# Optimization experiments

Measured on AMD Instinct MI355X. Metric: run time of the kernel, lower is better.

Reference implementation:

```python
import jax, jax.numpy as jnp
import numpy as np

B, N, G, E = 4, 8192, 512, 512
D = 3 * E  # fused channel dim = 1536
BN_EPS = 1e-5


def setup_inputs() -> dict:
    key = jax.random.key(0)
    ks = jax.random.split(key, 8)
    f32 = jnp.float32
    return {
        "xyz": jax.random.normal(ks[0], (B, N, 3), f32),
        "centers": jax.random.normal(ks[1], (B, G, 3), f32),
        "H4": jax.random.normal(ks[2], (B, G, E), f32),
        "H8": jax.random.normal(ks[3], (B, G, E), f32),
        "H12": jax.random.normal(ks[4], (B, G, E), f32),
        "w1": jax.random.normal(ks[5], (512, D), f32) * 0.02,
        "b1": jnp.zeros((512,), f32),
        "g1": jnp.ones((512,), f32),
        "be1": jnp.zeros((512,), f32),
        "m1": jnp.zeros((512,), f32),
        "v1": jnp.ones((512,), f32),
        "w2": jax.random.normal(ks[6], (512, 512), f32) * 0.02,
        "b2": jnp.zeros((512,), f32),
        "g2": jnp.ones((512,), f32),
        "be2": jnp.zeros((512,), f32),
        "m2": jnp.zeros((512,), f32),
        "v2": jnp.ones((512,), f32),
    }


def _bn(x, gamma, beta, mean, var):
    # BatchNorm1d, eval mode with running stats (per-channel, last axis)
    return (x - mean) * jax.lax.rsqrt(var + BN_EPS) * gamma + beta


def reference(xyz, centers, H4, H8, H12,
              w1, b1, g1, be1, m1, v1,
              w2, b2, g2, be2, m2, v2):
    fused = jnp.concatenate([H4, H8, H12], axis=-1)  # [B,G,D]
    # squared pairwise distances [B,N,G]
    d = (jnp.sum(xyz * xyz, axis=-1, keepdims=True)
         + jnp.sum(centers * centers, axis=-1)[:, None, :]
         - 2.0 * jnp.einsum('bnc,bgc->bng', xyz, centers))
    neg_d3, idx = jax.lax.top_k(-d, 3)  # 3 smallest distances, ascending
    d3 = -neg_d3  # [B,N,3]
    recip = 1.0 / (d3 + 1e-8)
    w = recip / jnp.sum(recip, axis=-1, keepdims=True)  # [B,N,3]
    # gather neighbor features: [B,N,3,D]
    gathered = jax.vmap(lambda f, i: f[i])(fused, idx)
    interp = jnp.einsum('bnk,bnkd->bnd', w, gathered)  # [B,N,D]
    # 1x1 conv == per-point linear; conv -> BN(eval) -> ReLU, twice
    h = jax.nn.relu(_bn(interp @ w1.T + b1, g1, be1, m1, v1))
    h = jax.nn.relu(_bn(h @ w2.T + b2, g2, be2, m2, v2))
    return h  # [B,N,512]
```

## Files before the change

kernel.cpp:

```cpp
#include <hip/hip_runtime.h>
#include <hip/hip_cooperative_groups.h>
#include <stdint.h>

#define NP 8192
#define NG 512
#define DF 1536

namespace cg = cooperative_groups;

using f32x4    = __attribute__((ext_vector_type(4))) float;
using bf16x8   = __attribute__((ext_vector_type(8))) __bf16;
using ushort8v = __attribute__((ext_vector_type(8))) unsigned short;


__device__ __forceinline__ unsigned short f32_to_bf16(float f) {
  unsigned int u = __float_as_uint(f);
  u += 0x7fffu + ((u >> 16) & 1u);
  return (unsigned short)(u >> 16);
}
__device__ __forceinline__ float bf2f(unsigned short u) {
  return __uint_as_float(((unsigned)u) << 16);
}

struct FusedArgs {
  const float *xyz, *centers, *H4, *H8, *H12, *w1, *w2;
  const float *g1, *be1, *m1, *v1, *g2, *be2, *m2, *v2, *b1, *b2;
  unsigned short *fswz, *w1s, *w2s, *Amatb;
  int *nidx; float *nw, *s1, *t1, *s2, *t2;
  float *outp;
};

__device__ void phase_setup(const FusedArgs& a, char* smem, int w) {
  const int tid = threadIdx.x;
  if (w < 512) {
    float4* cs = (float4*)smem;
    const int b = w >> 7;
    for (int i = tid; i < NG; i += 256) {
      float c0 = a.centers[((size_t)b * NG + i) * 3 + 0];
      float c1 = a.centers[((size_t)b * NG + i) * 3 + 1];
      float c2 = a.centers[((size_t)b * NG + i) * 3 + 2];
      float4 v; v.x = c0; v.y = c1; v.z = c2; v.w = c0 * c0 + c1 * c1 + c2 * c2;
      cs[(i >> 7) * 129 + (i & 127)] = v;
    }
    __syncthreads();
    const int t = (w & 127) * 256 + tid;
    const int p = t >> 2, q = t & 3;
    const size_t pi = (size_t)b * NP + p;
    const float x0 = a.xyz[pi * 3 + 0], x1 = a.xyz[pi * 3 + 1], x2 = a.xyz[pi * 3 + 2];
    const float xx = x0 * x0 + x1 * x1 + x2 * x2;
    float d0 = 3.4e38f, d1 = 3.4e38f, d2 = 3.4e38f;
    int i0 = 0, i1 = 0, i2 = 0;
    const int gbase = q * 128;
    const float4* csq = cs + q * 129;
#pragma unroll 4
    for (int j = 0; j < 128; ++j) {
      float4 c = csq[j];
      float d = xx + c.w - 2.0f * (x0 * c.x + x1 * c.y + x2 * c.z);
      int g = gbase + j;
      bool c0 = d < d0, c1 = d < d1, c2 = d < d2;
      float nd2 = c1 ? d1 : (c2 ? d : d2); int ni2 = c1 ? i1 : (c2 ? g : i2);
      float nd1 = c0 ? d0 : (c1 ? d : d1); int ni1 = c0 ? i0 : (c1 ? g : i1);
      d0 = c0 ? d : d0;                    i0 = c0 ? g : i0;
      d1 = nd1; i1 = ni1; d2 = nd2; i2 = ni2;
    }
#pragma unroll
    for (int off = 1; off <= 2; off <<= 1) {
      float e0 = __shfl_xor(d0, off), e1 = __shfl_xor(d1, off), e2 = __shfl_xor(d2, off);
      int j0 = __shfl_xor(i0, off), j1 = __shfl_xor(i1, off), j2 = __shfl_xor(i2, off);
#pragma unroll
      for (int s = 0; s < 3; ++s) {
        float e = (s == 0) ? e0 : (s == 1 ? e1 : e2);
        int   j = (s == 0) ? j0 : (s == 1 ? j1 : j2);
        bool c0 = (e < d0) || (e == d0 && j < i0);
        bool c1 = (e < d1) || (e == d1 && j < i1);
        bool c2 = (e < d2) || (e == d2 && j < i2);
        float nd2 = c1 ? d1 : (c2 ? e : d2); int ni2 = c1 ? i1 : (c2 ? j : i2);
        float nd1 = c0 ? d0 : (c1 ? e : d1); int ni1 = c0 ? i0 : (c1 ? j : i1);
        d0 = c0 ? e : d0;                    i0 = c0 ? j : i0;
        d1 = nd1; i1 = ni1; d2 = nd2; i2 = ni2;
      }
    }
    if (q == 0) {
      float r0 = 1.0f / (d0 + 1e-8f), r1 = 1.0f / (d1 + 1e-8f), r2 = 1.0f / (d2 + 1e-8f);
      float inv = 1.0f / (r0 + r1 + r2);
      a.nw[pi * 3 + 0] = r0 * inv; a.nw[pi * 3 + 1] = r1 * inv; a.nw[pi * 3 + 2] = r2 * inv;
      a.nidx[pi * 3 + 0] = i0; a.nidx[pi * 3 + 1] = i1; a.nidx[pi * 3 + 2] = i2;
    }
    __syncthreads();
  } else if (w < 2048) {
    const int qd = (w - 512) * 256 + tid;
    const int L = qd & 63, t2 = qd >> 6;
    const int kc = t2 % 48, mg = t2 / 48;
    const int m = mg * 16 + (L & 15);
    const int k = kc * 32 + (L >> 4) * 8;
    const float* src = (k < 512) ? a.H4 : (k < 1024 ? a.H8 : a.H12);
    const float* sp = &src[(size_t)m * 512 + (k & 511)];
    float4 va = *(const float4*)sp, vb = *(const float4*)(sp + 4);
    ushort8v o;
    o[0] = f32_to_bf16(va.x); o[1] = f32_to_bf16(va.y);
    o[2] = f32_to_bf16(va.z); o[3] = f32_to_bf16(va.w);
    o[4] = f32_to_bf16(vb.x); o[5] = f32_to_bf16(vb.y);
    o[6] = f32_to_bf16(vb.z); o[7] = f32_to_bf16(vb.w);
    *(ushort8v*)&a.fswz[((size_t)(mg * 48 + kc)) * 512 + L * 8] = o;
  } else if (w < 2432) {
    const int qd = (w - 2048) * 256 + tid;
    const int L = qd & 63, t2 = qd >> 6;
    const int kc = t2 % 48, ng = t2 / 48;
    const int n = ng * 16 + (L & 15);
    const int k = kc * 32 + (L >> 4) * 8;
    const float* sp = &a.w1[(size_t)n * 1536 + k];
    float4 va = *(const float4*)sp, vb = *(const float4*)(sp + 4);
    ushort8v o;
    o[0] = f32_to_bf16(va.x); o[1] = f32_to_bf16(va.y);
    o[2] = f32_to_bf16(va.z); o[3] = f32_to_bf16(va.w);
    o[4] = f32_to_bf16(vb.x); o[5] = f32_to_bf16(vb.y);
    o[6] = f32_to_bf16(vb.z); o[7] = f32_to_bf16(vb.w);
    *(ushort8v*)&a.w1s[((size_t)(ng * 48 + kc)) * 512 + L * 8] = o;
  } else if (w < 2560) {
    const int qd = (w - 2432) * 256 + tid;
    const int L = qd & 63, t2 = qd >> 6;
    const int kc = t2 & 15, ng = t2 >> 4;
    const int n = ng * 16 + (L & 15);
    const int k = kc * 32 + (L >> 4) * 8;
    const float* sp = &a.w2[(size_t)n * 512 + k];
    float4 va = *(const float4*)sp, vb = *(const float4*)(sp + 4);
    ushort8v o;
    o[0] = f32_to_bf16(va.x); o[1] = f32_to_bf16(va.y);
    o[2] = f32_to_bf16(va.z); o[3] = f32_to_bf16(va.w);
    o[4] = f32_to_bf16(vb.x); o[5] = f32_to_bf16(vb.y);
    o[6] = f32_to_bf16(vb.z); o[7] = f32_to_bf16(vb.w);
    *(ushort8v*)&a.w2s[((size_t)(ng * 16 + kc)) * 512 + L * 8] = o;
  } else {
    for (int i = tid; i < 512; i += 256) {
      float sa = a.g1[i] / sqrtf(a.v1[i] + 1e-5f);
      a.s1[i] = sa; a.t1[i] = a.be1[i] - a.m1[i] * sa;
      float sb = a.g2[i] / sqrtf(a.v2[i] + 1e-5f);
      a.s2[i] = sb; a.t2[i] = a.be2[i] - a.m2[i] * sb;
    }
  }
}

__device__ void phase_gemm1(const FusedArgs& a, char* smem) {
  float* red = (float*)smem;
  const int tid = threadIdx.x, lane = tid & 63, wv = tid >> 6;
  const int blk = blockIdx.x;
  const int m0 = (blk >> 3) * 32;
  const int n0 = (blk & 7) * 64;
  const unsigned short* Ap = a.fswz + ((size_t)(m0 >> 4) * 48 + wv * 12) * 512 + lane * 8;
  const unsigned short* Bp = a.w1s  + ((size_t)(n0 >> 4) * 48 + wv * 12) * 512 + lane * 8;

  f32x4 acc[2][4];
#pragma unroll
  for (int i = 0; i < 2; ++i)
#pragma unroll
    for (int j = 0; j < 4; ++j) acc[i][j] = (f32x4){0.f, 0.f, 0.f, 0.f};

  bf16x8 af[2], bfr[4], afn[2], bfn[4];
#pragma unroll
  for (int i = 0; i < 2; ++i)
    af[i]  = __builtin_bit_cast(bf16x8, *(const ushort8v*)(Ap + (size_t)i * 48 * 512));
#pragma unroll
  for (int i = 0; i < 4; ++i)
    bfr[i] = __builtin_bit_cast(bf16x8, *(const ushort8v*)(Bp + (size_t)i * 48 * 512));
#pragma unroll 1
  for (int kc = 0; kc < 12; ++kc) {
    if (kc < 11) {
#pragma unroll
      for (int i = 0; i < 2; ++i)
        afn[i] = __builtin_bit_cast(bf16x8, *(const ushort8v*)(Ap + (size_t)i * 48 * 512 + (kc + 1) * 512));
#pragma unroll
      for (int i = 0; i < 4; ++i)
        bfn[i] = __builtin_bit_cast(bf16x8, *(const ushort8v*)(Bp + (size_t)i * 48 * 512 + (kc + 1) * 512));
    }
#pragma unroll
    for (int mi = 0; mi < 2; ++mi)
#pragma unroll
      for (int ni = 0; ni < 4; ++ni)
        acc[mi][ni] = __builtin_amdgcn_mfma_f32_16x16x32_bf16(af[mi], bfr[ni], acc[mi][ni], 0, 0, 0);
#pragma unroll
    for (int i = 0; i < 2; ++i) af[i] = afn[i];
#pragma unroll
    for (int i = 0; i < 4; ++i) bfr[i] = bfn[i];
  }

  for (int w = 0; w < 4; ++w) {
    if (wv == w) {
#pragma unroll
      for (int mi = 0; mi < 2; ++mi)
#pragma unroll
        for (int ni = 0; ni < 4; ++ni) {
          int col = ni * 16 + (lane & 15);
#pragma unroll
          for (int r = 0; r < 4; ++r) {
            int row = mi * 16 + (lane >> 4) * 4 + r;
            if (w == 0) red[row * 65 + col] = acc[mi][ni][r];
            else        red[row * 65 + col] += acc[mi][ni][r];
          }
        }
    }
    __syncthreads();
  }
  const int row = tid >> 3;
  const int col = (tid & 7) * 8;
  ushort8v o;
#pragma unroll
  for (int j = 0; j < 8; ++j) {
    int n = n0 + col + j;
    float v = red[row * 65 + col + j];
    o[j] = f32_to_bf16(a.s1[n] * (v + a.b1[n]) + a.t1[n]);
  }
  *(ushort8v*)&a.Amatb[(size_t)(m0 + row) * 512 + n0 + col] = o;
  __syncthreads();
}

__device__ void phase_mega(const FusedArgs& a, char* smem) {
  unsigned short* hl = (unsigned short*)smem;
  const int tid = threadIdx.x, lane = tid & 63, wv = tid >> 6;
  const int xcd = blockIdx.x & 7, slot = blockIdx.x >> 3;
  const int m0 = (xcd * 64 + slot) * 64;

  {
    const int p = m0 + wv * 16 + (lane & 15);
    const int b = p >> 13;
    const int i0 = a.nidx[p * 3 + 0], i1 = a.nidx[p * 3 + 1], i2 = a.nidx[p * 3 + 2];
    const float w0 = a.nw[p * 3 + 0], w1v = a.nw[p * 3 + 1], w2v = a.nw[p * 3 + 2];
    const int co = (lane >> 4) * 8;
    const unsigned short* A0 = a.Amatb + ((size_t)(b * 512 + i0)) * 512 + co;
    const unsigned short* A1 = a.Amatb + ((size_t)(b * 512 + i1)) * 512 + co;
    const unsigned short* A2 = a.Amatb + ((size_t)(b * 512 + i2)) * 512 + co;
    unsigned short* wp = hl + (size_t)(wv * 16) * 512 + lane * 8;
#pragma unroll 4
    for (int kc = 0; kc < 16; ++kc) {
      ushort8v u0 = *(const ushort8v*)(A0 + kc * 32);
      ushort8v u1 = *(const ushort8v*)(A1 + kc * 32);
      ushort8v u2 = *(const ushort8v*)(A2 + kc * 32);
      ushort8v o;
#pragma unroll
      for (int j = 0; j < 8; ++j) {
        float v = w0 * bf2f(u0[j]) + w1v * bf2f(u1[j]) + w2v * bf2f(u2[j]);
        o[j] = f32_to_bf16(fmaxf(v, 0.f));
      }
      *(ushort8v*)(wp + (size_t)kc * 512) = o;
    }
  }
  __syncthreads();

  const int n0 = wv * 128;
  const unsigned short* Bbase = a.w2s + (size_t)(n0 >> 4) * 16 * 512 + lane * 8;

  f32x4 acc[4][8];
#pragma unroll
  for (int i = 0; i < 4; ++i)
#pragma unroll
    for (int j = 0; j < 8; ++j) acc[i][j] = (f32x4){0.f, 0.f, 0.f, 0.f};

#pragma unroll 1
  for (int kc = 0; kc < 16; ++kc) {
    bf16x8 af[4], bfr[8];
#pragma unroll
    for (int mi = 0; mi < 4; ++mi)
      af[mi] = __builtin_bit_cast(bf16x8,
          *(const ushort8v*)(hl + (size_t)(mi * 16 + kc) * 512 + lane * 8));
#pragma unroll
    for (int ni = 0; ni < 8; ++ni)
      bfr[ni] = __builtin_bit_cast(bf16x8,
          *(const ushort8v*)(Bbase + (size_t)(ni * 16 + kc) * 512));
#pragma unroll
    for (int mi = 0; mi < 4; ++mi)
#pragma unroll
      for (int ni = 0; ni < 8; ++ni)
        acc[mi][ni] = __builtin_amdgcn_mfma_f32_16x16x32_bf16(af[mi], bfr[ni], acc[mi][ni], 0, 0, 0);
  }

#pragma unroll
  for (int mi = 0; mi < 4; ++mi) {
    int mbase = m0 + mi * 16 + (lane >> 4) * 4;
#pragma unroll
    for (int ni = 0; ni < 8; ++ni) {
      int n = n0 + ni * 16 + (lane & 15);
      float s = a.s2[n], bb = a.b2[n], t = a.t2[n];
      f32x4 v = acc[mi][ni];
#pragma unroll
      for (int r = 0; r < 4; ++r)
        a.outp[(size_t)(mbase + r) * 512 + n] = fmaxf(s * (v[r] + bb) + t, 0.f);
    }
  }
}

__global__ __launch_bounds__(256, 2) void fused_kernel(FusedArgs a) {
  __shared__ __align__(16) char smem[65536];
  cg::grid_group grid = cg::this_grid();
  const int blk = blockIdx.x;
  for (int u = blk; u <= 2560; u += 512) phase_setup(a, smem, u);
  grid.sync();
  phase_gemm1(a, smem);
  grid.sync();
  phase_mega(a, smem);
}

__global__ __launch_bounds__(256) void k_setup(FusedArgs a) {
  __shared__ __align__(16) char smem[8448];
  for (int u = blockIdx.x; u <= 2560; u += 512) phase_setup(a, smem, u);
}
__global__ __launch_bounds__(256) void k_gemm1(FusedArgs a) {
  __shared__ __align__(16) char smem[8448];
  phase_gemm1(a, smem);
}
__global__ __launch_bounds__(256, 2) void k_mega(FusedArgs a) {
  __shared__ __align__(16) char smem[65536];
  phase_mega(a, smem);
}

extern "C" void kernel_launch(void* const* d_in, const int* in_sizes, int n_in,
                              void* d_out, int out_size, void* d_ws, size_t ws_size,
                              hipStream_t stream) {
  char* ws = (char*)d_ws;
  FusedArgs a;
  a.xyz     = (const float*)d_in[0];
  a.centers = (const float*)d_in[1];
  a.H4      = (const float*)d_in[2];
  a.H8      = (const float*)d_in[3];
  a.H12     = (const float*)d_in[4];
  a.w1      = (const float*)d_in[5];
  a.b1      = (const float*)d_in[6];
  a.g1      = (const float*)d_in[7];
  a.be1     = (const float*)d_in[8];
  a.m1      = (const float*)d_in[9];
  a.v1      = (const float*)d_in[10];
  a.w2      = (const float*)d_in[11];
  a.b2      = (const float*)d_in[12];
  a.g2      = (const float*)d_in[13];
  a.be2     = (const float*)d_in[14];
  a.m2      = (const float*)d_in[15];
  a.v2      = (const float*)d_in[16];
  a.fswz  = (unsigned short*)(ws);
  a.w1s   = (unsigned short*)(ws + 6291456);
  a.w2s   = (unsigned short*)(ws + 7864320);
  a.Amatb = (unsigned short*)(ws + 8388608);
  a.nidx  = (int*)           (ws + 10485760);
  a.nw    = (float*)         (ws + 10878976);
  a.s1    = (float*)         (ws + 11272192);
  a.t1 = a.s1 + 512; a.s2 = a.t1 + 512; a.t2 = a.s2 + 512;
  a.outp  = (float*)d_out;

  int nb = 0;
  hipError_t qerr = hipOccupancyMaxActiveBlocksPerMultiprocessor(
      &nb, reinterpret_cast<const void*>(fused_kernel), 256, 0);
  bool coop_ok = (qerr == hipSuccess) && (nb >= 2);
  if (coop_ok) {
    void* kp[] = { (void*)&a };
    hipError_t lerr = hipLaunchCooperativeKernel(
        (const void*)fused_kernel, dim3(512), dim3(256), kp, 0, stream);
    coop_ok = (lerr == hipSuccess);
  }
  if (!coop_ok) {
    k_setup <<<512, 256, 0, stream>>>(a);
    k_gemm1 <<<512, 256, 0, stream>>>(a);
    k_mega  <<<512, 256, 0, stream>>>(a);
  }
}
```

Before: 167.5 us.

## Overlap kNN with GEMM1 and double grid to 1024 blocks with smaller mega tiles

Moves the kNN search out of the setup phase so it runs alongside the first GEMM in a second phase, with each half of a 1024-block cooperative grid taking one of the two. The mega phase now handles 32 rows per block instead of 64, which halves its shared memory and accumulator footprint so launch bounds can ask for 4 blocks per CU. The cast work is spread over more blocks. The aim is to cut phase imbalance and raise occupancy. The cost is that each block reloads the W2 tiles for fewer rows, and 4 blocks per CU may push register pressure or fail the cooperative occupancy check, which would fall back to three separate launches.

```diff
diff --git a/kernel.cpp b/kernel.cpp
--- a/kernel.cpp
+++ b/kernel.cpp
@@ -11,6 +11,7 @@
 using f32x4    = __attribute__((ext_vector_type(4))) float;
 using bf16x8   = __attribute__((ext_vector_type(8))) __bf16;
 using ushort8v = __attribute__((ext_vector_type(8))) unsigned short;
+using ushort4v = __attribute__((ext_vector_type(4))) unsigned short;
 
 
 __device__ __forceinline__ unsigned short f32_to_bf16(float f) {
@@ -30,65 +31,68 @@
   float *outp;
 };
 
-__device__ void phase_setup(const FusedArgs& a, char* smem, int w) {
+__device__ void phase_knn(const FusedArgs& a, char* smem, int w) {
   const int tid = threadIdx.x;
-  if (w < 512) {
-    float4* cs = (float4*)smem;
-    const int b = w >> 7;
-    for (int i = tid; i < NG; i += 256) {
-      float c0 = a.centers[((size_t)b * NG + i) * 3 + 0];
-      float c1 = a.centers[((size_t)b * NG + i) * 3 + 1];
-      float c2 = a.centers[((size_t)b * NG + i) * 3 + 2];
-      float4 v; v.x = c0; v.y = c1; v.z = c2; v.w = c0 * c0 + c1 * c1 + c2 * c2;
-      cs[(i >> 7) * 129 + (i & 127)] = v;
-    }
-    __syncthreads();
-    const int t = (w & 127) * 256 + tid;
-    const int p = t >> 2, q = t & 3;
-    const size_t pi = (size_t)b * NP + p;
-    const float x0 = a.xyz[pi * 3 + 0], x1 = a.xyz[pi * 3 + 1], x2 = a.xyz[pi * 3 + 2];
-    const float xx = x0 * x0 + x1 * x1 + x2 * x2;
-    float d0 = 3.4e38f, d1 = 3.4e38f, d2 = 3.4e38f;
-    int i0 = 0, i1 = 0, i2 = 0;
-    const int gbase = q * 128;
-    const float4* csq = cs + q * 129;
+  float4* cs = (float4*)smem;
+  const int b = w >> 7;
+  for (int i = tid; i < NG; i += 256) {
+    float c0 = a.centers[((size_t)b * NG + i) * 3 + 0];
+    float c1 = a.centers[((size_t)b * NG + i) * 3 + 1];
+    float c2 = a.centers[((size_t)b * NG + i) * 3 + 2];
+    float4 v; v.x = c0; v.y = c1; v.z = c2; v.w = c0 * c0 + c1 * c1 + c2 * c2;
+    cs[(i >> 7) * 129 + (i & 127)] = v;
+  }
+  __syncthreads();
+  const int t = (w & 127) * 256 + tid;
+  const int p = t >> 2, q = t & 3;
+  const size_t pi = (size_t)b * NP + p;
+  const float x0 = a.xyz[pi * 3 + 0], x1 = a.xyz[pi * 3 + 1], x2 = a.xyz[pi * 3 + 2];
+  const float xx = x0 * x0 + x1 * x1 + x2 * x2;
+  float d0 = 3.4e38f, d1 = 3.4e38f, d2 = 3.4e38f;
+  int i0 = 0, i1 = 0, i2 = 0;
+  const int gbase = q * 128;
+  const float4* csq = cs + q * 129;
 #pragma unroll 4
-    for (int j = 0; j < 128; ++j) {
-      float4 c = csq[j];
-      float d = xx + c.w - 2.0f * (x0 * c.x + x1 * c.y + x2 * c.z);
-      int g = gbase + j;
-      bool c0 = d < d0, c1 = d < d1, c2 = d < d2;
-      float nd2 = c1 ? d1 : (c2 ? d : d2); int ni2 = c1 ? i1 : (c2 ? g : i2);
-      float nd1 = c0 ? d0 : (c1 ? d : d1); int ni1 = c0 ? i0 : (c1 ? g : i1);
-      d0 = c0 ? d : d0;                    i0 = c0 ? g : i0;
+  for (int j = 0; j < 128; ++j) {
+    float4 c = csq[j];
+    float d = xx + c.w - 2.0f * (x0 * c.x + x1 * c.y + x2 * c.z);
+    int g = gbase + j;
+    bool c0 = d < d0, c1 = d < d1, c2 = d < d2;
+    float nd2 = c1 ? d1 : (c2 ? d : d2); int ni2 = c1 ? i1 : (c2 ? g : i2);
+    float nd1 = c0 ? d0 : (c1 ? d : d1); int ni1 = c0 ? i0 : (c1 ? g : i1);
+    d0 = c0 ? d : d0;                    i0 = c0 ? g : i0;
+    d1 = nd1; i1 = ni1; d2 = nd2; i2 = ni2;
+  }
+#pragma unroll
+  for (int off = 1; off <= 2; off <<= 1) {
+    float e0 = __shfl_xor(d0, off), e1 = __shfl_xor(d1, off), e2 = __shfl_xor(d2, off);
+    int j0 = __shfl_xor(i0, off), j1 = __shfl_xor(i1, off), j2 = __shfl_xor(i2, off);
+#pragma unroll
+    for (int s = 0; s < 3; ++s) {
+      float e = (s == 0) ? e0 : (s == 1 ? e1 : e2);
+      int   j = (s == 0) ? j0 : (s == 1 ? j1 : j2);
+      bool c0 = (e < d0) || (e == d0 && j < i0);
+      bool c1 = (e < d1) || (e == d1 && j < i1);
+      bool c2 = (e < d2) || (e == d2 && j < i2);
+      float nd2 = c1 ? d1 : (c2 ? e : d2); int ni2 = c1 ? i1 : (c2 ? j : i2);
+      float nd1 = c0 ? d0 : (c1 ? e : d1); int ni1 = c0 ? i0 : (c1 ? j : i1);
+      d0 = c0 ? e : d0;                    i0 = c0 ? j : i0;
       d1 = nd1; i1 = ni1; d2 = nd2; i2 = ni2;
     }
-#pragma unroll
-    for (int off = 1; off <= 2; off <<= 1) {
-      float e0 = __shfl_xor(d0, off), e1 = __shfl_xor(d1, off), e2 = __shfl_xor(d2, off);
-      int j0 = __shfl_xor(i0, off), j1 = __shfl_xor(i1, off), j2 = __shfl_xor(i2, off);
-#pragma unroll
-      for (int s = 0; s < 3; ++s) {
-        float e = (s == 0) ? e0 : (s == 1 ? e1 : e2);
-        int   j = (s == 0) ? j0 : (s == 1 ? j1 : j2);
-        bool c0 = (e < d0) || (e == d0 && j < i0);
-        bool c1 = (e < d1) || (e == d1 && j < i1);
-        bool c2 = (e < d2) || (e == d2 && j < i2);
-        float nd2 = c1 ? d1 : (c2 ? e : d2); int ni2 = c1 ? i1 : (c2 ? j : i2);
-        float nd1 = c0 ? d0 : (c1 ? e : d1); int ni1 = c0 ? i0 : (c1 ? j : i1);
-        d0 = c0 ? e : d0;                    i0 = c0 ? j : i0;
-        d1 = nd1; i1 = ni1; d2 = nd2; i2 = ni2;
-      }
-    }
-    if (q == 0) {
-      float r0 = 1.0f / (d0 + 1e-8f), r1 = 1.0f / (d1 + 1e-8f), r2 = 1.0f / (d2 + 1e-8f);
-      float inv = 1.0f / (r0 + r1 + r2);
-      a.nw[pi * 3 + 0] = r0 * inv; a.nw[pi * 3 + 1] = r1 * inv; a.nw[pi * 3 + 2] = r2 * inv;
-      a.nidx[pi * 3 + 0] = i0; a.nidx[pi * 3 + 1] = i1; a.nidx[pi * 3 + 2] = i2;
-    }
-    __syncthreads();
-  } else if (w < 2048) {
-    const int qd = (w - 512) * 256 + tid;
+  }
+  if (q == 0) {
+    float r0 = 1.0f / (d0 + 1e-8f), r1 = 1.0f / (d1 + 1e-8f), r2 = 1.0f / (d2 + 1e-8f);
+    float inv = 1.0f / (r0 + r1 + r2);
+    a.nw[pi * 3 + 0] = r0 * inv; a.nw[pi * 3 + 1] = r1 * inv; a.nw[pi * 3 + 2] = r2 * inv;
+    a.nidx[pi * 3 + 0] = i0; a.nidx[pi * 3 + 1] = i1; a.nidx[pi * 3 + 2] = i2;
+  }
+  __syncthreads();
+}
+
+__device__ void phase_casts(const FusedArgs& a, int u) {
+  const int tid = threadIdx.x;
+  if (u < 2048) {
+    const int qd = (u - 512) * 256 + tid;
     const int L = qd & 63, t2 = qd >> 6;
     const int kc = t2 % 48, mg = t2 / 48;
     const int m = mg * 16 + (L & 15);
@@ -102,8 +106,8 @@
     o[4] = f32_to_bf16(vb.x); o[5] = f32_to_bf16(vb.y);
     o[6] = f32_to_bf16(vb.z); o[7] = f32_to_bf16(vb.w);
     *(ushort8v*)&a.fswz[((size_t)(mg * 48 + kc)) * 512 + L * 8] = o;
-  } else if (w < 2432) {
-    const int qd = (w - 2048) * 256 + tid;
+  } else if (u < 2432) {
+    const int qd = (u - 2048) * 256 + tid;
     const int L = qd & 63, t2 = qd >> 6;
     const int kc = t2 % 48, ng = t2 / 48;
     const int n = ng * 16 + (L & 15);
@@ -116,8 +120,8 @@
     o[4] = f32_to_bf16(vb.x); o[5] = f32_to_bf16(vb.y);
     o[6] = f32_to_bf16(vb.z); o[7] = f32_to_bf16(vb.w);
     *(ushort8v*)&a.w1s[((size_t)(ng * 48 + kc)) * 512 + L * 8] = o;
-  } else if (w < 2560) {
-    const int qd = (w - 2432) * 256 + tid;
+  } else if (u < 2560) {
+    const int qd = (u - 2432) * 256 + tid;
     const int L = qd & 63, t2 = qd >> 6;
     const int kc = t2 & 15, ng = t2 >> 4;
     const int n = ng * 16 + (L & 15);
@@ -140,10 +144,9 @@
   }
 }
 
-__device__ void phase_gemm1(const FusedArgs& a, char* smem) {
+__device__ void phase_gemm1(const FusedArgs& a, char* smem, int blk) {
   float* red = (float*)smem;
   const int tid = threadIdx.x, lane = tid & 63, wv = tid >> 6;
-  const int blk = blockIdx.x;
   const int m0 = (blk >> 3) * 32;
   const int n0 = (blk & 7) * 64;
   const unsigned short* Ap = a.fswz + ((size_t)(m0 >> 4) * 48 + wv * 12) * 512 + lane * 8;
@@ -217,30 +220,31 @@
   unsigned short* hl = (unsigned short*)smem;
   const int tid = threadIdx.x, lane = tid & 63, wv = tid >> 6;
   const int xcd = blockIdx.x & 7, slot = blockIdx.x >> 3;
-  const int m0 = (xcd * 64 + slot) * 64;
+  const int m0 = (xcd * 128 + slot) * 32;
 
   {
-    const int p = m0 + wv * 16 + (lane & 15);
+    const int rg = wv >> 1, kc0 = (wv & 1) * 8;
+    const int p = m0 + rg * 16 + (lane & 15);
     const int b = p >> 13;
     const int i0 = a.nidx[p * 3 + 0], i1 = a.nidx[p * 3 + 1], i2 = a.nidx[p * 3 + 2];
     const float w0 = a.nw[p * 3 + 0], w1v = a.nw[p * 3 + 1], w2v = a.nw[p * 3 + 2];
-    const int co = (lane >> 4) * 8;
+    const int co = kc0 * 32 + (lane >> 4) * 8;
     const unsigned short* A0 = a.Amatb + ((size_t)(b * 512 + i0)) * 512 + co;
     const unsigned short* A1 = a.Amatb + ((size_t)(b * 512 + i1)) * 512 + co;
     const unsigned short* A2 = a.Amatb + ((size_t)(b * 512 + i2)) * 512 + co;
-    unsigned short* wp = hl + (size_t)(wv * 16) * 512 + lane * 8;
+    unsigned short* wp = hl + (size_t)(rg * 16 + kc0) * 512 + lane * 8;
 #pragma unroll 4
-    for (int kc = 0; kc < 16; ++kc) {
-      ushort8v u0 = *(const ushort8v*)(A0 + kc * 32);
-      ushort8v u1 = *(const ushort8v*)(A1 + kc * 32);
-      ushort8v u2 = *(const ushort8v*)(A2 + kc * 32);
+    for (int j = 0; j < 8; ++j) {
+      ushort8v u0 = *(const ushort8v*)(A0 + j * 32);
+      ushort8v u1 = *(const ushort8v*)(A1 + j * 32);
+      ushort8v u2 = *(const ushort8v*)(A2 + j * 32);
       ushort8v o;
 #pragma unroll
-      for (int j = 0; j < 8; ++j) {
-        float v = w0 * bf2f(u0[j]) + w1v * bf2f(u1[j]) + w2v * bf2f(u2[j]);
-        o[j] = f32_to_bf16(fmaxf(v, 0.f));
+      for (int jj = 0; jj < 8; ++jj) {
+        float v = w0 * bf2f(u0[jj]) + w1v * bf2f(u1[jj]) + w2v * bf2f(u2[jj]);
+        o[jj] = f32_to_bf16(fmaxf(v, 0.f));
       }
-      *(ushort8v*)(wp + (size_t)kc * 512) = o;
+      *(ushort8v*)(wp + (size_t)j * 512) = o;
     }
   }
   __syncthreads();
@@ -248,32 +252,37 @@
   const int n0 = wv * 128;
   const unsigned short* Bbase = a.w2s + (size_t)(n0 >> 4) * 16 * 512 + lane * 8;
 
-  f32x4 acc[4][8];
-#pragma unroll
-  for (int i = 0; i < 4; ++i)
+  f32x4 acc[2][8];
+#pragma unroll
+  for (int i = 0; i < 2; ++i)
 #pragma unroll
     for (int j = 0; j < 8; ++j) acc[i][j] = (f32x4){0.f, 0.f, 0.f, 0.f};
 
 #pragma unroll 1
   for (int kc = 0; kc < 16; ++kc) {
-    bf16x8 af[4], bfr[8];
-#pragma unroll
-    for (int mi = 0; mi < 4; ++mi)
+    bf16x8 af[2];
+#pragma unroll
+    for (int mi = 0; mi < 2; ++mi)
       af[mi] = __builtin_bit_cast(bf16x8,
           *(const ushort8v*)(hl + (size_t)(mi * 16 + kc) * 512 + lane * 8));
 #pragma unroll
-    for (int ni = 0; ni < 8; ++ni)
-      bfr[ni] = __builtin_bit_cast(bf16x8,
-          *(const ushort8v*)(Bbase + (size_t)(ni * 16 + kc) * 512));
-#pragma unroll
-    for (int mi = 0; mi < 4; ++mi)
-#pragma unroll
-      for (int ni = 0; ni < 8; ++ni)
-        acc[mi][ni] = __builtin_amdgcn_mfma_f32_16x16x32_bf16(af[mi], bfr[ni], acc[mi][ni], 0, 0, 0);
-  }
-
-#pragma unroll
-  for (int mi = 0; mi < 4; ++mi) {
+    for (int h = 0; h < 2; ++h) {
+      bf16x8 bfr[4];
+#pragma unroll
+      for (int ni = 0; ni < 4; ++ni)
+        bfr[ni] = __builtin_bit_cast(bf16x8,
+            *(const ushort8v*)(Bbase + (size_t)((h * 4 + ni) * 16 + kc) * 512));
+#pragma unroll
+      for (int mi = 0; mi < 2; ++mi)
+#pragma unroll
+        for (int ni = 0; ni < 4; ++ni)
+          acc[mi][h * 4 + ni] = __builtin_amdgcn_mfma_f32_16x16x32_bf16(
+              af[mi], bfr[ni], acc[mi][h * 4 + ni], 0, 0, 0);
+    }
+  }
+
+#pragma unroll
+  for (int mi = 0; mi < 2; ++mi) {
     int mbase = m0 + mi * 16 + (lane >> 4) * 4;
 #pragma unroll
     for (int ni = 0; ni < 8; ++ni) {
@@ -287,27 +296,28 @@
   }
 }
 
-__global__ __launch_bounds__(256, 2) void fused_kernel(FusedArgs a) {
-  __shared__ __align__(16) char smem[65536];
+__global__ __launch_bounds__(256, 4) void fused_kernel(FusedArgs a) {
+  __shared__ __align__(16) char smem[32768];
   cg::grid_group grid = cg::this_grid();
   const int blk = blockIdx.x;
-  for (int u = blk; u <= 2560; u += 512) phase_setup(a, smem, u);
+  for (int u = 512 + blk; u <= 2560; u += 1024) phase_casts(a, u);
   grid.sync();
-  phase_gemm1(a, smem);
+  if (blk < 512) phase_knn(a, smem, blk);
+  else           phase_gemm1(a, smem, blk - 512);
   grid.sync();
   phase_mega(a, smem);
 }
 
-__global__ __launch_bounds__(256) void k_setup(FusedArgs a) {
+__global__ __launch_bounds__(256) void k_setupA(FusedArgs a) {
+  for (int u = 512 + blockIdx.x; u <= 2560; u += 1024) phase_casts(a, u);
+}
+__global__ __launch_bounds__(256) void k_phaseB(FusedArgs a) {
   __shared__ __align__(16) char smem[8448];
-  for (int u = blockIdx.x; u <= 2560; u += 512) phase_setup(a, smem, u);
-}
-__global__ __launch_bounds__(256) void k_gemm1(FusedArgs a) {
-  __shared__ __align__(16) char smem[8448];
-  phase_gemm1(a, smem);
-}
-__global__ __launch_bounds__(256, 2) void k_mega(FusedArgs a) {
-  __shared__ __align__(16) char smem[65536];
+  if (blockIdx.x < 512) phase_knn(a, smem, blockIdx.x);
+  else                  phase_gemm1(a, smem, blockIdx.x - 512);
+}
+__global__ __launch_bounds__(256, 4) void k_mega(FusedArgs a) {
+  __shared__ __align__(16) char smem[32768];
   phase_mega(a, smem);
 }
 
@@ -346,16 +356,16 @@
   int nb = 0;
   hipError_t qerr = hipOccupancyMaxActiveBlocksPerMultiprocessor(
       &nb, reinterpret_cast<const void*>(fused_kernel), 256, 0);
-  bool coop_ok = (qerr == hipSuccess) && (nb >= 2);
+  bool coop_ok = (qerr == hipSuccess) && (nb >= 4);
   if (coop_ok) {
     void* kp[] = { (void*)&a };
     hipError_t lerr = hipLaunchCooperativeKernel(
-        (const void*)fused_kernel, dim3(512), dim3(256), kp, 0, stream);
+        (const void*)fused_kernel, dim3(1024), dim3(256), kp, 0, stream);
     coop_ok = (lerr == hipSuccess);
   }
   if (!coop_ok) {
-    k_setup <<<512, 256, 0, stream>>>(a);
-    k_gemm1 <<<512, 256, 0, stream>>>(a);
-    k_mega  <<<512, 256, 0, stream>>>(a);
-  }
-}
+    k_setupA<<<1024, 256, 0, stream>>>(a);
+    k_phaseB<<<1024, 256, 0, stream>>>(a);
+    k_mega  <<<1024, 256, 0, stream>>>(a);
+  }
+}
```

Result: no change. 167.8 us (+0.2%).
